# Kernel tuning notes

Hardware: AMD Instinct MI355X
Metric: run time of the kernel (lower is better)

## Reference

```python
import jax, jax.numpy as jnp
import numpy as np

DEGREE = 8
TAU = 2.0
EPS = 1e-5
V_TH = 1.0


def chebyshev_basis(x, degree):
    # x: [b, i] -> [b, i, degree+1]
    xn = jnp.tanh(0.5 * x)
    T = [jnp.ones_like(xn), xn]
    for _ in range(2, degree + 1):
        T.append(2.0 * xn * T[-1] - T[-2])
    return jnp.stack(T, axis=-1)


def spike_fn(v):
    # single-step LIF from zero state: heaviside at threshold
    return (v >= V_TH).astype(v.dtype)


def skan_layer(x, coeffs, scale, gamma, beta):
    basis = chebyshev_basis(x, DEGREE)            # [b, i, d]
    h = jnp.einsum('bid,oid->bo', basis, coeffs) * scale
    # BatchNorm1d (training-mode batch stats, biased variance)
    mu = jnp.mean(h, axis=0)
    var = jnp.var(h, axis=0)
    h = gamma * (h - mu) * jax.lax.rsqrt(var + EPS) + beta
    # LIF: mem starts at 0 -> mem = mem + (h - mem)/tau = h/tau
    mem = h / TAU
    return spike_fn(mem)


def _kan_coeffs(key, out_f, in_f, degree):
    c = jnp.zeros((out_f, in_f, degree + 1), jnp.float32)
    c = c.at[:, :, 1].set(1.0 / in_f)
    c = c.at[:, :, 2:].set(0.01 * jax.random.normal(key, (out_f, in_f, degree - 1), jnp.float32))
    return c


def setup_inputs() -> dict:
    key = jax.random.key(0)
    ks = jax.random.split(key, 5)
    B, IN, H1, H2, NC = 1024, 1024, 2048, 1024, 1000
    x = jax.random.normal(ks[0], (B, IN), jnp.float32)
    coeffs1 = _kan_coeffs(ks[1], H1, IN, DEGREE)
    scale1 = jnp.ones((H1,), jnp.float32)
    gamma1 = jnp.ones((H1,), jnp.float32)
    beta1 = jnp.zeros((H1,), jnp.float32)
    coeffs2 = _kan_coeffs(ks[2], H2, H1, DEGREE)
    scale2 = jnp.ones((H2,), jnp.float32)
    gamma2 = jnp.ones((H2,), jnp.float32)
    beta2 = jnp.zeros((H2,), jnp.float32)
    lim = 1.0 / np.sqrt(H2)
    w = jax.random.uniform(ks[3], (NC, H2), jnp.float32, -lim, lim)
    b = jax.random.uniform(ks[4], (NC,), jnp.float32, -lim, lim)
    return {"x": x, "coeffs1": coeffs1, "scale1": scale1, "gamma1": gamma1,
            "beta1": beta1, "coeffs2": coeffs2, "scale2": scale2,
            "gamma2": gamma2, "beta2": beta2, "w": w, "b": b}


def reference(x, coeffs1, scale1, gamma1, beta1, coeffs2, scale2, gamma2, beta2, w, b):
    s1 = skan_layer(x, coeffs1, scale1, gamma1, beta1)
    s2 = skan_layer(s1, coeffs2, scale2, gamma2, beta2)
    out = s2 @ w.T + b
    return (out, s1, s2)
```

## Files before the change

kernel.cpp:

```cpp
#include <hip/hip_runtime.h>
#include <math.h>

#define NB 9

static constexpr int BATCH = 1024;
static constexpr int IN1   = 1024;
static constexpr int HID1  = 2048;
static constexpr int HID2  = 1024;
static constexpr int NCLS  = 1000;
static constexpr int K1    = IN1 * NB;

typedef double double4v __attribute__((ext_vector_type(4)));

__global__ __launch_bounds__(256)
void k_xnT(const float* __restrict__ x, double* __restrict__ xnT) {
  const int i = blockIdx.x;
  const int b = blockIdx.y * 256 + threadIdx.x;
  xnT[(size_t)i * BATCH + b] = tanh(0.5 * (double)x[(size_t)b * IN1 + i]);
}

__device__ __forceinline__ double fA(int l) {
  return (double)((l & 15) + 17 * (l >> 4));
}
__device__ __forceinline__ double gB(int l) {
  return (double)((l & 15) * (l & 15) + 3 * (l >> 4));
}

__global__ void k_probe(int* __restrict__ flag) {
  const int l = threadIdx.x;
  double4v acc = {0.0, 0.0, 0.0, 0.0};
  acc = __builtin_amdgcn_mfma_f64_16x16x4f64(fA(l), gB(l), acc, 0, 0, 0);
  bool ok[16];
#pragma unroll
  for (int c = 0; c < 16; ++c) ok[c] = true;
  for (int dopt = 0; dopt < 4; ++dopt) {
    for (int r = 0; r < 4; ++r) {
      int q = (dopt < 2) ? (4 * (l >> 4) + r) : ((l >> 4) + 4 * r);
      int i = (dopt == 0 || dopt == 2) ? q : (l & 15);
      int j = (dopt == 0 || dopt == 2) ? (l & 15) : q;
      double v = acc[r];
      for (int ao = 0; ao < 2; ++ao)
        for (int bo = 0; bo < 2; ++bo) {
          double p = 0.0;
          for (int k = 0; k < 4; ++k) {
            int la = ao ? (4 * i + k) : (i + 16 * k);
            int lb = bo ? (4 * j + k) : (j + 16 * k);
            p += fA(la) * gB(lb);
          }
          if (v != p) ok[ao * 8 + bo * 4 + dopt] = false;
        }
    }
  }
  int res = 16;
  for (int c = 15; c >= 0; --c)
    if (__ballot(ok[c]) == ~0ull) res = c;
  if (l == 0) flag[0] = res;
}

__global__ __launch_bounds__(256)
void k_gemm1_mfma(const double* __restrict__ xnT, const float* __restrict__ cf,
                  const int* __restrict__ flag, double* __restrict__ h1) {
  const int fl = flag[0];
  if (fl >= 16) return;
  const int ao = fl >> 3, bo = (fl >> 2) & 1, dopt = fl & 3;
  __shared__ float  lA[2][36][130];
  __shared__ double lB[2][36][66];
  const int tid  = threadIdx.x;
  const int lane = tid & 63;
  const int w    = tid >> 6;
  const int wo   = (w & 1) * 64;
  const int wb   = (w >> 1) * 32;
  const int o0   = blockIdx.y * 128;
  const int b0   = blockIdx.x * 64;
  const int l15  = lane & 15;
  const int l4   = lane >> 4;
  const int am = ao ? (lane >> 2) : l15;
  const int ak = ao ? (lane & 3)  : l4;
  const int bn = bo ? (lane >> 2) : l15;
  const int bk = bo ? (lane & 3)  : l4;
  const int soo = tid >> 1, sk0 = (tid & 1) * 18;
  const int sbb = tid & 63, sii = tid >> 6;

  double4v acc[4][2];
#pragma unroll
  for (int m = 0; m < 4; ++m)
#pragma unroll
    for (int n = 0; n < 2; ++n) acc[m][n] = double4v{0.0, 0.0, 0.0, 0.0};

  const float* abase = cf + (size_t)(o0 + soo) * K1 + sk0;
  float2 creg[9];
  double xv;
  {
    const float2* src = (const float2*)abase;
#pragma unroll
    for (int q = 0; q < 9; ++q) creg[q] = src[q];
    xv = xnT[(size_t)sii * BATCH + b0 + sbb];
  }
  int cur = 0;
  for (int ic = 0; ic < 256; ++ic) {
#pragma unroll
    for (int q = 0; q < 9; ++q) {
      lA[cur][sk0 + 2 * q][soo]     = creg[q].x;
      lA[cur][sk0 + 2 * q + 1][soo] = creg[q].y;
    }
    {
      double t0 = 1.0, t1 = xv;
      lB[cur][sii * NB + 0][sbb] = t0;
      lB[cur][sii * NB + 1][sbb] = t1;
#pragma unroll
      for (int d = 2; d < NB; ++d) {
        double t2 = 2.0 * xv * t1 - t0;
        lB[cur][sii * NB + d][sbb] = t2;
        t0 = t1; t1 = t2;
      }
    }
    __syncthreads();
    if (ic < 255) {
      const int i0 = (ic + 1) * 4;
      const float2* src = (const float2*)(abase + (size_t)i0 * NB);
#pragma unroll
      for (int q = 0; q < 9; ++q) creg[q] = src[q];
      xv = xnT[(size_t)(i0 + sii) * BATCH + b0 + sbb];
    }
#pragma unroll
    for (int k4 = 0; k4 < 9; ++k4) {
      double a[4], b[2];
#pragma unroll
      for (int m = 0; m < 4; ++m)
        a[m] = (double)lA[cur][k4 * 4 + ak][wo + m * 16 + am];
#pragma unroll
      for (int n = 0; n < 2; ++n)
        b[n] = lB[cur][k4 * 4 + bk][wb + n * 16 + bn];
#pragma unroll
      for (int m = 0; m < 4; ++m)
#pragma unroll
        for (int n = 0; n < 2; ++n)
          acc[m][n] =
              __builtin_amdgcn_mfma_f64_16x16x4f64(a[m], b[n], acc[m][n], 0, 0, 0);
    }
    cur ^= 1;
  }
#pragma unroll
  for (int m = 0; m < 4; ++m)
#pragma unroll
    for (int n = 0; n < 2; ++n) {
      const int ob = o0 + wo + m * 16;
      const int bb = b0 + wb + n * 16;
      if (dopt == 0) {
        int o = ob + 4 * l4, b = bb + l15;
#pragma unroll
        for (int j = 0; j < 4; ++j)
          h1[(size_t)(o + j) * BATCH + b] = acc[m][n][j];
      } else if (dopt == 1) {
        int o = ob + l15, b = bb + 4 * l4;
#pragma unroll
        for (int j = 0; j < 4; ++j)
          h1[(size_t)o * BATCH + b + j] = acc[m][n][j];
      } else if (dopt == 2) {
        int o = ob + l4, b = bb + l15;
#pragma unroll
        for (int j = 0; j < 4; ++j)
          h1[(size_t)(o + 4 * j) * BATCH + b] = acc[m][n][j];
      } else {
        int o = ob + l15, b = bb + l4;
#pragma unroll
        for (int j = 0; j < 4; ++j)
          h1[(size_t)o * BATCH + b + 4 * j] = acc[m][n][j];
      }
    }
}

__global__ __launch_bounds__(256)
void k_gemm1_valu(const double* __restrict__ xnT, const float* __restrict__ cf,
                  const int* __restrict__ flag, double* __restrict__ h1) {
  if (flag[0] != 16) return;
  __shared__ double lbas[4][64][NB];
  __shared__ double lcf[4][NB][65];
  const int tx = threadIdx.x & 15;
  const int ty = threadIdx.x >> 4;
  const int b0 = blockIdx.x * 64;
  const int o0 = blockIdx.y * 64;
  double acc[4][4];
#pragma unroll
  for (int i = 0; i < 4; ++i)
#pragma unroll
    for (int j = 0; j < 4; ++j) acc[i][j] = 0.0;

  for (int i0 = 0; i0 < IN1; i0 += 4) {
    {
      int e = threadIdx.x;
      int bb = e & 63, ii = e >> 6;
      double v = xnT[(size_t)(i0 + ii) * BATCH + b0 + bb];
      double t0 = 1.0, t1 = v;
      lbas[ii][bb][0] = t0;
      lbas[ii][bb][1] = t1;
#pragma unroll
      for (int d = 2; d < NB; ++d) {
        double t2 = 2.0 * v * t1 - t0;
        lbas[ii][bb][d] = t2;
        t0 = t1; t1 = t2;
      }
    }
    for (int e = threadIdx.x; e < 64 * 36; e += 256) {
      int oo = e / 36;
      int r  = e - oo * 36;
      int ii = r / NB;
      int d  = r - ii * NB;
      lcf[ii][d][oo] =
          (double)cf[(size_t)(o0 + oo) * K1 + (size_t)(i0 + ii) * NB + d];
    }
    __syncthreads();
#pragma unroll
    for (int ii = 0; ii < 4; ++ii) {
#pragma unroll
      for (int d = 0; d < NB; ++d) {
        double bs[4], cv[4];
#pragma unroll
        for (int r = 0; r < 4; ++r) bs[r] = lbas[ii][tx + 16 * r][d];
#pragma unroll
        for (int r = 0; r < 4; ++r) cv[r] = lcf[ii][d][ty + 16 * r];
#pragma unroll
        for (int ro = 0; ro < 4; ++ro)
#pragma unroll
          for (int rb = 0; rb < 4; ++rb)
            acc[rb][ro] = fma(bs[rb], cv[ro], acc[rb][ro]);
      }
    }
    __syncthreads();
  }
#pragma unroll
  for (int ro = 0; ro < 4; ++ro)
#pragma unroll
    for (int rb = 0; rb < 4; ++rb)
      h1[(size_t)(o0 + ty + 16 * ro) * BATCH + b0 + tx + 16 * rb] = acc[rb][ro];
}

__global__ __launch_bounds__(256)
void k_bnstats(const double* __restrict__ h, const float* __restrict__ scale,
               const float* __restrict__ gamma, const float* __restrict__ beta,
               double* __restrict__ AC, int batch) {
  const int f = blockIdx.x;
  const double* row = h + (size_t)f * batch;
  double s1 = 0.0, s2 = 0.0;
  for (int b = threadIdx.x; b < batch; b += 256) {
    double v = row[b];
    s1 += v;
    s2 = fma(v, v, s2);
  }
#pragma unroll
  for (int off = 32; off > 0; off >>= 1) {
    s1 += __shfl_down(s1, off, 64);
    s2 += __shfl_down(s2, off, 64);
  }
  __shared__ double red[8];
  const int wid = threadIdx.x >> 6;
  if ((threadIdx.x & 63) == 0) { red[wid] = s1; red[4 + wid] = s2; }
  __syncthreads();
  if (threadIdx.x == 0) {
    double S1 = red[0] + red[1] + red[2] + red[3];
    double S2 = red[4] + red[5] + red[6] + red[7];
    double m1 = S1 / batch;
    double m2 = S2 / batch;
    double sc = (double)scale[f], g = (double)gamma[f], be = (double)beta[f];
    double var = sc * sc * (m2 - m1 * m1);
    double inv = 1.0 / sqrt(var + 1e-5);
    double A = g * sc * inv;
    double C = be - g * sc * m1 * inv;
    AC[2 * f] = A;
    AC[2 * f + 1] = C;
  }
}

__global__ __launch_bounds__(256)
void k_spike_tr(const double* __restrict__ h, const double* __restrict__ AC,
                float* __restrict__ s, int batch, int F) {
  __shared__ float tile[64][65];
  __shared__ double lA[64], lC[64];
  const int b0 = blockIdx.x * 64;
  const int f0 = blockIdx.y * 64;
  const int t = threadIdx.x;
  if (t < 64) { lA[t] = AC[2 * (f0 + t)]; lC[t] = AC[2 * (f0 + t) + 1]; }
  __syncthreads();
  const int tx = t & 63, tw = t >> 6;
  for (int fo = tw; fo < 64; fo += 4) {
    double v = h[(size_t)(f0 + fo) * batch + b0 + tx];
    tile[tx][fo] = (fma(lA[fo], v, lC[fo]) >= 2.0) ? 1.0f : 0.0f;
  }
  __syncthreads();
  for (int bo = tw; bo < 64; bo += 4) {
    s[(size_t)(b0 + bo) * F + f0 + tx] = tile[bo][tx];
  }
}

__global__ __launch_bounds__(256)
void k_prep2(const float* __restrict__ cf2, double* __restrict__ a2,
             double* __restrict__ c0v) {
  const int o = blockIdx.x;
  double bt[NB], b0a[NB];
  {
    double tt = tanh(0.5);
    bt[0] = 1.0; bt[1] = tt;
    b0a[0] = 1.0; b0a[1] = 0.0;
#pragma unroll
    for (int d = 2; d < NB; ++d) {
      bt[d] = 2.0 * tt * bt[d - 1] - bt[d - 2];
      b0a[d] = -b0a[d - 2];
    }
  }
  double cp = 0.0;
  for (int i = threadIdx.x; i < HID1; i += 256) {
    const float* c = cf2 + ((size_t)o * HID1 + i) * NB;
    double av = 0.0, cv = 0.0;
#pragma unroll
    for (int d = 0; d < NB; ++d) {
      double cd = (double)c[d];
      av = fma(bt[d] - b0a[d], cd, av);
      cv = fma(b0a[d], cd, cv);
    }
    a2[(size_t)o * HID1 + i] = av;
    cp += cv;
  }
#pragma unroll
  for (int off = 32; off > 0; off >>= 1) cp += __shfl_down(cp, off, 64);
  __shared__ double red[4];
  if ((threadIdx.x & 63) == 0) red[threadIdx.x >> 6] = cp;
  __syncthreads();
  if (threadIdx.x == 0) c0v[o] = red[0] + red[1] + red[2] + red[3];
}

__global__ __launch_bounds__(256)
void k_gemm2_mfma(const float* __restrict__ s1, const double* __restrict__ a2,
                  const double* __restrict__ c0v, const int* __restrict__ flag,
                  double* __restrict__ h2) {
  const int fl = flag[0];
  if (fl >= 16) return;
  const int ao = fl >> 3, bo = (fl >> 2) & 1, dopt = fl & 3;
  __shared__ double lA[2][32][66];
  __shared__ float  lB[2][32][66];
  const int tid  = threadIdx.x;
  const int lane = tid & 63;
  const int w    = tid >> 6;
  const int wo   = (w & 1) * 32;
  const int wb   = (w >> 1) * 32;
  const int o0   = blockIdx.y * 64;
  const int b0   = blockIdx.x * 64;
  const int l15  = lane & 15;
  const int l4   = lane >> 4;
  const int am = ao ? (lane >> 2) : l15;
  const int ak = ao ? (lane & 3)  : l4;
  const int bn = bo ? (lane >> 2) : l15;
  const int bk = bo ? (lane & 3)  : l4;
  const int srow = tid >> 2, sk = (tid & 3) * 8;

  double4v acc[2][2];
#pragma unroll
  for (int m = 0; m < 2; ++m)
#pragma unroll
    for (int n = 0; n < 2; ++n) acc[m][n] = double4v{0.0, 0.0, 0.0, 0.0};

  const double* Abase = a2 + (size_t)(o0 + srow) * HID1 + sk;
  const float*  Bbase = s1 + (size_t)(b0 + srow) * HID1 + sk;
  double areg[8];
  float  breg[8];
#pragma unroll
  for (int q = 0; q < 8; ++q) areg[q] = Abase[q];
#pragma unroll
  for (int q = 0; q < 8; ++q) breg[q] = Bbase[q];

  int cur = 0;
  for (int t = 0; t < HID1 / 32; ++t) {
#pragma unroll
    for (int q = 0; q < 8; ++q) lA[cur][sk + q][srow] = areg[q];
#pragma unroll
    for (int q = 0; q < 8; ++q) lB[cur][sk + q][srow] = breg[q];
    __syncthreads();
    if (t < HID1 / 32 - 1) {
      const int i0 = (t + 1) * 32;
#pragma unroll
      for (int q = 0; q < 8; ++q) areg[q] = Abase[i0 + q];
#pragma unroll
      for (int q = 0; q < 8; ++q) breg[q] = Bbase[i0 + q];
    }
#pragma unroll
    for (int k4 = 0; k4 < 8; ++k4) {
      double a[2], b[2];
#pragma unroll
      for (int m = 0; m < 2; ++m)
        a[m] = lA[cur][k4 * 4 + ak][wo + m * 16 + am];
#pragma unroll
      for (int n = 0; n < 2; ++n)
        b[n] = (double)lB[cur][k4 * 4 + bk][wb + n * 16 + bn];
#pragma unroll
      for (int m = 0; m < 2; ++m)
#pragma unroll
        for (int n = 0; n < 2; ++n)
          acc[m][n] =
              __builtin_amdgcn_mfma_f64_16x16x4f64(a[m], b[n], acc[m][n], 0, 0, 0);
    }
    cur ^= 1;
  }
#pragma unroll
  for (int m = 0; m < 2; ++m)
#pragma unroll
    for (int n = 0; n < 2; ++n) {
      const int ob = o0 + wo + m * 16;
      const int bb = b0 + wb + n * 16;
      if (dopt == 0) {
        int o = ob + 4 * l4, b = bb + l15;
#pragma unroll
        for (int j = 0; j < 4; ++j)
          h2[(size_t)(o + j) * BATCH + b] = acc[m][n][j] + c0v[o + j];
      } else if (dopt == 1) {
        int o = ob + l15, b = bb + 4 * l4;
        double c0 = c0v[o];
#pragma unroll
        for (int j = 0; j < 4; ++j)
          h2[(size_t)o * BATCH + b + j] = acc[m][n][j] + c0;
      } else if (dopt == 2) {
        int o = ob + l4, b = bb + l15;
#pragma unroll
        for (int j = 0; j < 4; ++j)
          h2[(size_t)(o + 4 * j) * BATCH + b] = acc[m][n][j] + c0v[o + 4 * j];
      } else {
        int o = ob + l15, b = bb + l4;
        double c0 = c0v[o];
#pragma unroll
        for (int j = 0; j < 4; ++j)
          h2[(size_t)o * BATCH + b + 4 * j] = acc[m][n][j] + c0;
      }
    }
}

__global__ __launch_bounds__(256)
void k_gemm2_valu(const float* __restrict__ s1, const double* __restrict__ a2,
                  const double* __restrict__ c0v, const int* __restrict__ flag,
                  double* __restrict__ h2) {
  if (flag[0] != 16) return;
  __shared__ double ls[16][64];
  __shared__ double la[16][32];
  const int tx = threadIdx.x & 15;
  const int ty = threadIdx.x >> 4;
  const int b0 = blockIdx.x * 64;
  const int o0 = blockIdx.y * 32;
  double acc[4][2] = {{0, 0}, {0, 0}, {0, 0}, {0, 0}};
  for (int i0 = 0; i0 < HID1; i0 += 16) {
    for (int e = threadIdx.x; e < 64 * 16; e += 256) {
      int bb = e & 63, ii = e >> 6;
      ls[ii][bb] = (double)s1[(size_t)(b0 + bb) * HID1 + i0 + ii];
    }
    for (int e = threadIdx.x; e < 32 * 16; e += 256) {
      int oo = e & 31, ii = e >> 5;
      la[ii][oo] = a2[(size_t)(o0 + oo) * HID1 + i0 + ii];
    }
    __syncthreads();
#pragma unroll
    for (int ii = 0; ii < 16; ++ii) {
      double sv[4], av[2];
#pragma unroll
      for (int r = 0; r < 4; ++r) sv[r] = ls[ii][tx + 16 * r];
      av[0] = la[ii][ty];
      av[1] = la[ii][ty + 16];
#pragma unroll
      for (int ro = 0; ro < 2; ++ro)
#pragma unroll
        for (int rb = 0; rb < 4; ++rb)
          acc[rb][ro] = fma(sv[rb], av[ro], acc[rb][ro]);
    }
    __syncthreads();
  }
#pragma unroll
  for (int ro = 0; ro < 2; ++ro) {
    double c0 = c0v[o0 + ty + 16 * ro];
#pragma unroll
    for (int rb = 0; rb < 4; ++rb)
      h2[(size_t)(o0 + ty + 16 * ro) * BATCH + b0 + tx + 16 * rb] =
          acc[rb][ro] + c0;
  }
}

__global__ __launch_bounds__(256)
void k_gemm3(const float* __restrict__ s2, const float* __restrict__ w,
             const float* __restrict__ bias, float* __restrict__ out) {
  __shared__ float lsS[32][64];
  __shared__ float lw[32][64];
  const int tx = threadIdx.x & 15;
  const int ty = threadIdx.x >> 4;
  const int b0 = blockIdx.x * 64;
  const int n0 = blockIdx.y * 64;
  float acc[4][4];
#pragma unroll
  for (int i = 0; i < 4; ++i)
#pragma unroll
    for (int j = 0; j < 4; ++j) acc[i][j] = 0.0f;
  for (int k0 = 0; k0 < HID2; k0 += 32) {
    for (int e = threadIdx.x; e < 64 * 32; e += 256) {
      int bb = e & 63, kk = e >> 6;
      lsS[kk][bb] = s2[(size_t)(b0 + bb) * HID2 + k0 + kk];
    }
    for (int e = threadIdx.x; e < 64 * 32; e += 256) {
      int nn = e & 63, kk = e >> 6;
      int n = n0 + nn;
      lw[kk][nn] = (n < NCLS) ? w[(size_t)n * HID2 + k0 + kk] : 0.0f;
    }
    __syncthreads();
#pragma unroll
    for (int kk = 0; kk < 32; ++kk) {
      float sv[4], wv[4];
#pragma unroll
      for (int r = 0; r < 4; ++r) sv[r] = lsS[kk][ty + 16 * r];
#pragma unroll
      for (int r = 0; r < 4; ++r) wv[r] = lw[kk][tx + 16 * r];
#pragma unroll
      for (int rb = 0; rb < 4; ++rb)
#pragma unroll
        for (int rn = 0; rn < 4; ++rn)
          acc[rb][rn] = fmaf(sv[rb], wv[rn], acc[rb][rn]);
    }
    __syncthreads();
  }
#pragma unroll
  for (int rn = 0; rn < 4; ++rn) {
    int n = n0 + tx + 16 * rn;
    if (n < NCLS) {
      float bv = bias[n];
#pragma unroll
      for (int rb = 0; rb < 4; ++rb)
        out[(size_t)(b0 + ty + 16 * rb) * NCLS + n] = acc[rb][rn] + bv;
    }
  }
}

extern "C" void kernel_launch(void* const* d_in, const int* in_sizes, int n_in,
                              void* d_out, int out_size, void* d_ws,
                              size_t ws_size, hipStream_t stream) {
  (void)in_sizes; (void)n_in; (void)out_size; (void)ws_size;
  const float* x       = (const float*)d_in[0];
  const float* coeffs1 = (const float*)d_in[1];
  const float* scale1  = (const float*)d_in[2];
  const float* gamma1  = (const float*)d_in[3];
  const float* beta1   = (const float*)d_in[4];
  const float* coeffs2 = (const float*)d_in[5];
  const float* scale2  = (const float*)d_in[6];
  const float* gamma2  = (const float*)d_in[7];
  const float* beta2   = (const float*)d_in[8];
  const float* w       = (const float*)d_in[9];
  const float* bias    = (const float*)d_in[10];

  float* out = (float*)d_out;
  float* s1  = out + (size_t)BATCH * NCLS;
  float* s2  = s1 + (size_t)BATCH * HID1;

  char* ws = (char*)d_ws;
  int*    flag = (int*)ws;   ws += 16;
  double* xnT  = (double*)ws; ws += (size_t)IN1 * BATCH * 8;
  double* h1   = (double*)ws; ws += (size_t)HID1 * BATCH * 8;
  double* AC1  = (double*)ws; ws += (size_t)HID1 * 2 * 8;
  double* a2   = (double*)ws; ws += (size_t)HID2 * HID1 * 8;
  double* c0v  = (double*)ws; ws += (size_t)HID2 * 8;
  double* h2   = (double*)ws; ws += (size_t)HID2 * BATCH * 8;
  double* AC2  = (double*)ws; ws += (size_t)HID2 * 2 * 8;

  k_xnT<<<dim3(IN1, BATCH / 256), 256, 0, stream>>>(x, xnT);
  k_probe<<<1, 64, 0, stream>>>(flag);
  k_prep2<<<HID2, 256, 0, stream>>>(coeffs2, a2, c0v);
  k_gemm1_mfma<<<dim3(BATCH / 64, HID1 / 128), 256, 0, stream>>>(xnT, coeffs1,
                                                                 flag, h1);
  k_gemm1_valu<<<dim3(BATCH / 64, HID1 / 64), 256, 0, stream>>>(xnT, coeffs1,
                                                                flag, h1);
  k_bnstats<<<HID1, 256, 0, stream>>>(h1, scale1, gamma1, beta1, AC1, BATCH);
  k_spike_tr<<<dim3(BATCH / 64, HID1 / 64), 256, 0, stream>>>(h1, AC1, s1,
                                                              BATCH, HID1);
  k_gemm2_mfma<<<dim3(BATCH / 64, HID2 / 64), 256, 0, stream>>>(s1, a2, c0v,
                                                                flag, h2);
  k_gemm2_valu<<<dim3(BATCH / 64, HID2 / 32), 256, 0, stream>>>(s1, a2, c0v,
                                                                flag, h2);
  k_bnstats<<<HID2, 256, 0, stream>>>(h2, scale2, gamma2, beta2, AC2, BATCH);
  k_spike_tr<<<dim3(BATCH / 64, HID2 / 64), 256, 0, stream>>>(h2, AC2, s2,
                                                              BATCH, HID2);
  k_gemm3<<<dim3(BATCH / 64, 1024 / 64), 256, 0, stream>>>(s2, w, bias, out);
}
```

Baseline: 1.281 ms.

## Fold constant Chebyshev term out of GEMM1, retile GEMMs, add transposed spike output

```diff
diff --git a/kernel.cpp b/kernel.cpp
--- a/kernel.cpp
+++ b/kernel.cpp
@@ -14,9 +14,20 @@
 
 __global__ __launch_bounds__(256)
 void k_xnT(const float* __restrict__ x, double* __restrict__ xnT) {
-  const int i = blockIdx.x;
-  const int b = blockIdx.y * 256 + threadIdx.x;
-  xnT[(size_t)i * BATCH + b] = tanh(0.5 * (double)x[(size_t)b * IN1 + i]);
+  __shared__ double t[32][33];
+  const int i0 = blockIdx.x * 32, b0 = blockIdx.y * 32;
+  const int tx = threadIdx.x & 31, ty = threadIdx.x >> 5;
+#pragma unroll
+  for (int r = 0; r < 4; ++r) {
+    int bl = ty + 8 * r;
+    t[tx][bl] = tanh(0.5 * (double)x[(size_t)(b0 + bl) * IN1 + i0 + tx]);
+  }
+  __syncthreads();
+#pragma unroll
+  for (int r = 0; r < 4; ++r) {
+    int il = ty + 8 * r;
+    xnT[(size_t)(i0 + il) * BATCH + b0 + tx] = t[il][tx];
+  }
 }
 
 __device__ __forceinline__ double fA(int l) {
@@ -57,115 +68,132 @@
   if (l == 0) flag[0] = res;
 }
 
+__global__ __launch_bounds__(64)
+void k_prep1(const float* __restrict__ cf, double* __restrict__ c1c) {
+  const int o = blockIdx.x;
+  double s = 0.0;
+  for (int i = threadIdx.x; i < IN1; i += 64)
+    s += (double)cf[(size_t)o * K1 + (size_t)i * NB];
+#pragma unroll
+  for (int off = 32; off > 0; off >>= 1) s += __shfl_down(s, off, 64);
+  if (threadIdx.x == 0) c1c[o] = s;
+}
+
 __global__ __launch_bounds__(256)
 void k_gemm1_mfma(const double* __restrict__ xnT, const float* __restrict__ cf,
-                  const int* __restrict__ flag, double* __restrict__ h1) {
+                  const double* __restrict__ c1c, const int* __restrict__ flag,
+                  double* __restrict__ h1) {
   const int fl = flag[0];
   if (fl >= 16) return;
   const int ao = fl >> 3, bo = (fl >> 2) & 1, dopt = fl & 3;
-  __shared__ float  lA[2][36][130];
-  __shared__ double lB[2][36][66];
+  __shared__ float  lA[2][32][136];
+  __shared__ double lB[2][32][35];
   const int tid  = threadIdx.x;
   const int lane = tid & 63;
   const int w    = tid >> 6;
-  const int wo   = (w & 1) * 64;
-  const int wb   = (w >> 1) * 32;
+  const int wo   = w * 32;
   const int o0   = blockIdx.y * 128;
-  const int b0   = blockIdx.x * 64;
+  const int b0   = blockIdx.x * 32;
   const int l15  = lane & 15;
   const int l4   = lane >> 4;
   const int am = ao ? (lane >> 2) : l15;
   const int ak = ao ? (lane & 3)  : l4;
   const int bn = bo ? (lane >> 2) : l15;
   const int bk = bo ? (lane & 3)  : l4;
-  const int soo = tid >> 1, sk0 = (tid & 1) * 18;
-  const int sbb = tid & 63, sii = tid >> 6;
-
-  double4v acc[4][2];
-#pragma unroll
-  for (int m = 0; m < 4; ++m)
+  const int soo = tid >> 1, si2 = (tid & 1) * 2;
+  const int sbb = tid & 31, sii = (tid >> 5) & 3;
+
+  double4v acc[2][2];
+#pragma unroll
+  for (int m = 0; m < 2; ++m)
 #pragma unroll
     for (int n = 0; n < 2; ++n) acc[m][n] = double4v{0.0, 0.0, 0.0, 0.0};
 
-  const float* abase = cf + (size_t)(o0 + soo) * K1 + sk0;
-  float2 creg[9];
-  double xv;
-  {
-    const float2* src = (const float2*)abase;
-#pragma unroll
-    for (int q = 0; q < 9; ++q) creg[q] = src[q];
-    xv = xnT[(size_t)sii * BATCH + b0 + sbb];
-  }
+  const float* abase = cf + (size_t)(o0 + soo) * K1;
+  float c16[16];
+  double xv = 0.0;
+#pragma unroll
+  for (int j2 = 0; j2 < 2; ++j2)
+#pragma unroll
+    for (int d = 0; d < 8; ++d)
+      c16[j2 * 8 + d] = abase[(size_t)(si2 + j2) * NB + 1 + d];
+  if (tid < 128) xv = xnT[(size_t)sii * BATCH + b0 + sbb];
+
   int cur = 0;
   for (int ic = 0; ic < 256; ++ic) {
 #pragma unroll
-    for (int q = 0; q < 9; ++q) {
-      lA[cur][sk0 + 2 * q][soo]     = creg[q].x;
-      lA[cur][sk0 + 2 * q + 1][soo] = creg[q].y;
-    }
-    {
+    for (int j2 = 0; j2 < 2; ++j2)
+#pragma unroll
+      for (int d = 0; d < 8; ++d)
+        lA[cur][si2 * 8 + j2 * 8 + d][soo] = c16[j2 * 8 + d];
+    if (tid < 128) {
       double t0 = 1.0, t1 = xv;
-      lB[cur][sii * NB + 0][sbb] = t0;
-      lB[cur][sii * NB + 1][sbb] = t1;
+      lB[cur][sii * 8 + 0][sbb] = t1;
 #pragma unroll
       for (int d = 2; d < NB; ++d) {
         double t2 = 2.0 * xv * t1 - t0;
-        lB[cur][sii * NB + d][sbb] = t2;
+        lB[cur][sii * 8 + d - 1][sbb] = t2;
         t0 = t1; t1 = t2;
       }
     }
     __syncthreads();
     if (ic < 255) {
-      const int i0 = (ic + 1) * 4;
-      const float2* src = (const float2*)(abase + (size_t)i0 * NB);
-#pragma unroll
-      for (int q = 0; q < 9; ++q) creg[q] = src[q];
-      xv = xnT[(size_t)(i0 + sii) * BATCH + b0 + sbb];
-    }
-#pragma unroll
-    for (int k4 = 0; k4 < 9; ++k4) {
-      double a[4], b[2];
-#pragma unroll
-      for (int m = 0; m < 4; ++m)
+      const int i0n = (ic + 1) * 4;
+#pragma unroll
+      for (int j2 = 0; j2 < 2; ++j2)
+#pragma unroll
+        for (int d = 0; d < 8; ++d)
+          c16[j2 * 8 + d] = abase[(size_t)(i0n + si2 + j2) * NB + 1 + d];
+      if (tid < 128) xv = xnT[(size_t)(i0n + sii) * BATCH + b0 + sbb];
+    }
+    __builtin_amdgcn_s_setprio(1);
+#pragma unroll
+    for (int k4 = 0; k4 < 8; ++k4) {
+      double a[2], b[2];
+#pragma unroll
+      for (int m = 0; m < 2; ++m)
         a[m] = (double)lA[cur][k4 * 4 + ak][wo + m * 16 + am];
 #pragma unroll
       for (int n = 0; n < 2; ++n)
-        b[n] = lB[cur][k4 * 4 + bk][wb + n * 16 + bn];
-#pragma unroll
-      for (int m = 0; m < 4; ++m)
+        b[n] = lB[cur][k4 * 4 + bk][n * 16 + bn];
+#pragma unroll
+      for (int m = 0; m < 2; ++m)
 #pragma unroll
         for (int n = 0; n < 2; ++n)
           acc[m][n] =
               __builtin_amdgcn_mfma_f64_16x16x4f64(a[m], b[n], acc[m][n], 0, 0, 0);
     }
+    __builtin_amdgcn_s_setprio(0);
     cur ^= 1;
   }
 #pragma unroll
-  for (int m = 0; m < 4; ++m)
+  for (int m = 0; m < 2; ++m)
 #pragma unroll
     for (int n = 0; n < 2; ++n) {
       const int ob = o0 + wo + m * 16;
-      const int bb = b0 + wb + n * 16;
+      const int bb = b0 + n * 16;
       if (dopt == 0) {
         int o = ob + 4 * l4, b = bb + l15;
 #pragma unroll
         for (int j = 0; j < 4; ++j)
-          h1[(size_t)(o + j) * BATCH + b] = acc[m][n][j];
+          h1[(size_t)(o + j) * BATCH + b] = acc[m][n][j] + c1c[o + j];
       } else if (dopt == 1) {
         int o = ob + l15, b = bb + 4 * l4;
+        double cc = c1c[o];
 #pragma unroll
         for (int j = 0; j < 4; ++j)
-          h1[(size_t)o * BATCH + b + j] = acc[m][n][j];
+          h1[(size_t)o * BATCH + b + j] = acc[m][n][j] + cc;
       } else if (dopt == 2) {
         int o = ob + l4, b = bb + l15;
 #pragma unroll
         for (int j = 0; j < 4; ++j)
-          h1[(size_t)(o + 4 * j) * BATCH + b] = acc[m][n][j];
+          h1[(size_t)(o + 4 * j) * BATCH + b] = acc[m][n][j] + c1c[o + 4 * j];
       } else {
         int o = ob + l15, b = bb + l4;
+        double cc = c1c[o];
 #pragma unroll
         for (int j = 0; j < 4; ++j)
-          h1[(size_t)o * BATCH + b + 4 * j] = acc[m][n][j];
+          h1[(size_t)o * BATCH + b + 4 * j] = acc[m][n][j] + cc;
       }
     }
 }
@@ -273,7 +301,8 @@
 
 __global__ __launch_bounds__(256)
 void k_spike_tr(const double* __restrict__ h, const double* __restrict__ AC,
-                float* __restrict__ s, int batch, int F) {
+                float* __restrict__ s, float* __restrict__ sT, int batch,
+                int F) {
   __shared__ float tile[64][65];
   __shared__ double lA[64], lC[64];
   const int b0 = blockIdx.x * 64;
@@ -290,6 +319,9 @@
   for (int bo = tw; bo < 64; bo += 4) {
     s[(size_t)(b0 + bo) * F + f0 + tx] = tile[bo][tx];
   }
+  for (int fo = tw; fo < 64; fo += 4) {
+    sT[(size_t)(f0 + fo) * batch + b0 + tx] = tile[tx][fo];
+  }
 }
 
 __global__ __launch_bounds__(256)
@@ -329,106 +361,97 @@
 }
 
 __global__ __launch_bounds__(256)
-void k_gemm2_mfma(const float* __restrict__ s1, const double* __restrict__ a2,
+void k_gemm2_mfma(const float* __restrict__ s1T, const double* __restrict__ a2,
                   const double* __restrict__ c0v, const int* __restrict__ flag,
                   double* __restrict__ h2) {
   const int fl = flag[0];
   if (fl >= 16) return;
   const int ao = fl >> 3, bo = (fl >> 2) & 1, dopt = fl & 3;
-  __shared__ double lA[2][32][66];
-  __shared__ float  lB[2][32][66];
+  __shared__ double lA[2][32][67];
+  __shared__ float  lB[2][32][40];
   const int tid  = threadIdx.x;
   const int lane = tid & 63;
   const int w    = tid >> 6;
   const int wo   = (w & 1) * 32;
-  const int wb   = (w >> 1) * 32;
+  const int wb   = (w >> 1) * 16;
   const int o0   = blockIdx.y * 64;
-  const int b0   = blockIdx.x * 64;
+  const int b0   = blockIdx.x * 32;
   const int l15  = lane & 15;
   const int l4   = lane >> 4;
   const int am = ao ? (lane >> 2) : l15;
   const int ak = ao ? (lane & 3)  : l4;
   const int bn = bo ? (lane >> 2) : l15;
   const int bk = bo ? (lane & 3)  : l4;
-  const int srow = tid >> 2, sk = (tid & 3) * 8;
-
-  double4v acc[2][2];
-#pragma unroll
-  for (int m = 0; m < 2; ++m)
-#pragma unroll
-    for (int n = 0; n < 2; ++n) acc[m][n] = double4v{0.0, 0.0, 0.0, 0.0};
-
-  const double* Abase = a2 + (size_t)(o0 + srow) * HID1 + sk;
-  const float*  Bbase = s1 + (size_t)(b0 + srow) * HID1 + sk;
-  double areg[8];
-  float  breg[8];
-#pragma unroll
-  for (int q = 0; q < 8; ++q) areg[q] = Abase[q];
-#pragma unroll
-  for (int q = 0; q < 8; ++q) breg[q] = Bbase[q];
+  const int srA = tid >> 2, skA = (tid & 3) * 8;
+  const int srB = tid >> 3, scB = (tid & 7) * 4;
+
+  double4v acc[2];
+  acc[0] = double4v{0.0, 0.0, 0.0, 0.0};
+  acc[1] = double4v{0.0, 0.0, 0.0, 0.0};
+
+  const double* Abase = a2 + (size_t)(o0 + srA) * HID1 + skA;
+  const float*  Bbase = s1T + b0 + scB;
+  double ar[8];
+  float4 br;
+#pragma unroll
+  for (int q = 0; q < 8; ++q) ar[q] = Abase[q];
+  br = *(const float4*)(Bbase + (size_t)srB * BATCH);
 
   int cur = 0;
   for (int t = 0; t < HID1 / 32; ++t) {
 #pragma unroll
-    for (int q = 0; q < 8; ++q) lA[cur][sk + q][srow] = areg[q];
-#pragma unroll
-    for (int q = 0; q < 8; ++q) lB[cur][sk + q][srow] = breg[q];
+    for (int q = 0; q < 8; ++q) lA[cur][skA + q][srA] = ar[q];
+    *(float4*)&lB[cur][srB][scB] = br;
     __syncthreads();
     if (t < HID1 / 32 - 1) {
       const int i0 = (t + 1) * 32;
 #pragma unroll
-      for (int q = 0; q < 8; ++q) areg[q] = Abase[i0 + q];
-#pragma unroll
-      for (int q = 0; q < 8; ++q) breg[q] = Bbase[i0 + q];
-    }
+      for (int q = 0; q < 8; ++q) ar[q] = Abase[i0 + q];
+      br = *(const float4*)(Bbase + (size_t)(i0 + srB) * BATCH);
+    }
+    __builtin_amdgcn_s_setprio(1);
 #pragma unroll
     for (int k4 = 0; k4 < 8; ++k4) {
-      double a[2], b[2];
+      double a[2], b;
 #pragma unroll
       for (int m = 0; m < 2; ++m)
         a[m] = lA[cur][k4 * 4 + ak][wo + m * 16 + am];
-#pragma unroll
-      for (int n = 0; n < 2; ++n)
-        b[n] = (double)lB[cur][k4 * 4 + bk][wb + n * 16 + bn];
+      b = (double)lB[cur][k4 * 4 + bk][wb + bn];
 #pragma unroll
       for (int m = 0; m < 2; ++m)
-#pragma unroll
-        for (int n = 0; n < 2; ++n)
-          acc[m][n] =
-              __builtin_amdgcn_mfma_f64_16x16x4f64(a[m], b[n], acc[m][n], 0, 0, 0);
-    }
+        acc[m] = __builtin_amdgcn_mfma_f64_16x16x4f64(a[m], b, acc[m], 0, 0, 0);
+    }
+    __builtin_amdgcn_s_setprio(0);
     cur ^= 1;
   }
 #pragma unroll
-  for (int m = 0; m < 2; ++m)
-#pragma unroll
-    for (int n = 0; n < 2; ++n) {
-      const int ob = o0 + wo + m * 16;
-      const int bb = b0 + wb + n * 16;
-      if (dopt == 0) {
-        int o = ob + 4 * l4, b = bb + l15;
-#pragma unroll
-        for (int j = 0; j < 4; ++j)
-          h2[(size_t)(o + j) * BATCH + b] = acc[m][n][j] + c0v[o + j];
-      } else if (dopt == 1) {
-        int o = ob + l15, b = bb + 4 * l4;
-        double c0 = c0v[o];
-#pragma unroll
-        for (int j = 0; j < 4; ++j)
-          h2[(size_t)o * BATCH + b + j] = acc[m][n][j] + c0;
-      } else if (dopt == 2) {
-        int o = ob + l4, b = bb + l15;
-#pragma unroll
-        for (int j = 0; j < 4; ++j)
-          h2[(size_t)(o + 4 * j) * BATCH + b] = acc[m][n][j] + c0v[o + 4 * j];
-      } else {
-        int o = ob + l15, b = bb + l4;
-        double c0 = c0v[o];
-#pragma unroll
-        for (int j = 0; j < 4; ++j)
-          h2[(size_t)o * BATCH + b + 4 * j] = acc[m][n][j] + c0;
-      }
-    }
+  for (int m = 0; m < 2; ++m) {
+    const int ob = o0 + wo + m * 16;
+    const int bb = b0 + wb;
+    if (dopt == 0) {
+      int o = ob + 4 * l4, b = bb + l15;
+#pragma unroll
+      for (int j = 0; j < 4; ++j)
+        h2[(size_t)(o + j) * BATCH + b] = acc[m][j] + c0v[o + j];
+    } else if (dopt == 1) {
+      int o = ob + l15, b = bb + 4 * l4;
+      double c0 = c0v[o];
+#pragma unroll
+      for (int j = 0; j < 4; ++j)
+        h2[(size_t)o * BATCH + b + j] = acc[m][j] + c0;
+    } else if (dopt == 2) {
+      int o = ob + l4, b = bb + l15;
+#pragma unroll
+      for (int j = 0; j < 4; ++j)
+        h2[(size_t)(o + 4 * j) * BATCH + b] = acc[m][j] + c0v[o + 4 * j];
+    } else {
+      int o = ob + l15, b = bb + l4;
+      double c0 = c0v[o];
+#pragma unroll
+      for (int j = 0; j < 4; ++j)
+        h2[(size_t)o * BATCH + b + 4 * j] = acc[m][j] + c0;
+    }
+  }
 }
 
 __global__ __launch_bounds__(256)
@@ -551,7 +574,7 @@
   float* s2  = s1 + (size_t)BATCH * HID1;
 
   char* ws = (char*)d_ws;
-  int*    flag = (int*)ws;   ws += 16;
+  int*    flag = (int*)ws;    ws += 16;
   double* xnT  = (double*)ws; ws += (size_t)IN1 * BATCH * 8;
   double* h1   = (double*)ws; ws += (size_t)HID1 * BATCH * 8;
   double* AC1  = (double*)ws; ws += (size_t)HID1 * 2 * 8;
@@ -559,23 +582,28 @@
   double* c0v  = (double*)ws; ws += (size_t)HID2 * 8;
   double* h2   = (double*)ws; ws += (size_t)HID2 * BATCH * 8;
   double* AC2  = (double*)ws; ws += (size_t)HID2 * 2 * 8;
-
-  k_xnT<<<dim3(IN1, BATCH / 256), 256, 0, stream>>>(x, xnT);
+  double* c1c  = (double*)ws; ws += (size_t)HID1 * 8;
+
+  float* s1T = (float*)xnT;
+  float* s2T = (float*)h1;
+
+  k_xnT<<<dim3(IN1 / 32, BATCH / 32), 256, 0, stream>>>(x, xnT);
   k_probe<<<1, 64, 0, stream>>>(flag);
+  k_prep1<<<HID1, 64, 0, stream>>>(coeffs1, c1c);
   k_prep2<<<HID2, 256, 0, stream>>>(coeffs2, a2, c0v);
-  k_gemm1_mfma<<<dim3(BATCH / 64, HID1 / 128), 256, 0, stream>>>(xnT, coeffs1,
-                                                                 flag, h1);
+  k_gemm1_mfma<<<dim3(BATCH / 32, HID1 / 128), 256, 0, stream>>>(
+      xnT, coeffs1, c1c, flag, h1);
   k_gemm1_valu<<<dim3(BATCH / 64, HID1 / 64), 256, 0, stream>>>(xnT, coeffs1,
                                                                 flag, h1);
   k_bnstats<<<HID1, 256, 0, stream>>>(h1, scale1, gamma1, beta1, AC1, BATCH);
-  k_spike_tr<<<dim3(BATCH / 64, HID1 / 64), 256, 0, stream>>>(h1, AC1, s1,
+  k_spike_tr<<<dim3(BATCH / 64, HID1 / 64), 256, 0, stream>>>(h1, AC1, s1, s1T,
                                                               BATCH, HID1);
-  k_gemm2_mfma<<<dim3(BATCH / 64, HID2 / 64), 256, 0, stream>>>(s1, a2, c0v,
+  k_gemm2_mfma<<<dim3(BATCH / 32, HID2 / 64), 256, 0, stream>>>(s1T, a2, c0v,
                                                                 flag, h2);
   k_gemm2_valu<<<dim3(BATCH / 64, HID2 / 32), 256, 0, stream>>>(s1, a2, c0v,
                                                                 flag, h2);
   k_bnstats<<<HID2, 256, 0, stream>>>(h2, scale2, gamma2, beta2, AC2, BATCH);
-  k_spike_tr<<<dim3(BATCH / 64, HID2 / 64), 256, 0, stream>>>(h2, AC2, s2,
+  k_spike_tr<<<dim3(BATCH / 64, HID2 / 64), 256, 0, stream>>>(h2, AC2, s2, s2T,
                                                               BATCH, HID2);
   k_gemm3<<<dim3(BATCH / 64, 1024 / 64), 256, 0, stream>>>(s2, w, bias, out);
 }
```

New measurement: 1.126 ms. 1.14x faster.
